# Kernel tuning notes

Measured on AMD Instinct MI355X. Metric: run time of the kernel, lower is better.

## Reference

```python
import jax, jax.numpy as jnp
import numpy as np
from functools import partial

N_QUBITS = 8
DEPTH = 2
INPUT_DIM = 128
HIDDEN_DIM = N_QUBITS  # required: hx = o * tanh(cx) elementwise
DIM = 2 ** N_QUBITS

# Z expectation matrix: ZMAT[k, i] = +1/-1 depending on bit of basis state k at wire i
# (wire 0 is the most-significant qubit, PennyLane convention)
_bits = ((np.arange(DIM)[:, None] >> (N_QUBITS - 1 - np.arange(N_QUBITS)[None, :])) & 1)
ZMAT = jnp.asarray(1.0 - 2.0 * _bits, dtype=jnp.float32)  # [2**n, n]


def _apply_1q(state, G, wire):
    """Apply 2x2 gate G ([2,2] shared or [B,2,2] batched) on `wire`."""
    B = state.shape[0]
    left, right = 2 ** wire, 2 ** (N_QUBITS - wire - 1)
    s = state.reshape(B, left, 2, right)
    if G.ndim == 2:
        s = jnp.einsum('ij,bljr->blir', G, s)
    else:
        s = jnp.einsum('bij,bljr->blir', G, s)
    return s.reshape(B, DIM)


def _apply_cnot(state, wire):
    """CNOT with control=wire, target=wire+1 (adjacent)."""
    B = state.shape[0]
    left, right = 2 ** wire, 2 ** (N_QUBITS - wire - 2)
    s = state.reshape(B, left, 2, 2, right)
    s = jnp.concatenate([s[:, :, :1], s[:, :, 1:, ::-1]], axis=2)
    return s.reshape(B, DIM)


def quantum_gate(angles, params):
    """angles: [B, n] RX rotation angles; params: [depth, n] RY angles.
    Returns [B, n] PauliZ expectations (exact statevector simulation)."""
    B = angles.shape[0]
    state = jnp.zeros((B, DIM), dtype=jnp.complex64).at[:, 0].set(1.0)
    # RX encoding layer (batched angles)
    c = jnp.cos(angles / 2).astype(jnp.complex64)
    s = (-1j) * jnp.sin(angles / 2).astype(jnp.complex64)
    for i in range(N_QUBITS):
        G = jnp.stack([jnp.stack([c[:, i], s[:, i]], -1),
                       jnp.stack([s[:, i], c[:, i]], -1)], -2)  # [B,2,2]
        state = _apply_1q(state, G, i)
    # variational layers: RY (shared params) + CNOT chain
    cp = jnp.cos(params / 2).astype(jnp.complex64)
    sp = jnp.sin(params / 2).astype(jnp.complex64)
    for d in range(DEPTH):
        for i in range(N_QUBITS):
            G = jnp.array([[1.0, 0.0], [0.0, 1.0]], jnp.complex64)
            G = jnp.stack([jnp.stack([cp[d, i], -sp[d, i]]),
                           jnp.stack([sp[d, i], cp[d, i]])])  # [2,2]
            state = _apply_1q(state, G, i)
        for i in range(N_QUBITS - 1):
            state = _apply_cnot(state, i)
    probs = (state.real ** 2 + state.imag ** 2)  # [B, 2**n]
    return probs @ ZMAT  # [B, n]


def setup_inputs() -> dict:
    key = jax.random.key(0)
    ks = jax.random.split(key, 13)
    T, B = 256, 1024
    cat = INPUT_DIM + HIDDEN_DIM
    lin_scale = 1.0 / np.sqrt(cat)
    d = {'inputs': jax.random.normal(ks[0], (T, B, INPUT_DIM), jnp.float32)}
    for idx, g in enumerate(['f', 'i', 'g', 'o']):
        d[f'W{g}'] = jax.random.uniform(ks[1 + 3 * idx], (N_QUBITS, cat), jnp.float32, -lin_scale, lin_scale)
        d[f'b{g}'] = jax.random.uniform(ks[2 + 3 * idx], (N_QUBITS,), jnp.float32, -lin_scale, lin_scale)
        d[f'P{g}'] = jax.random.normal(ks[3 + 3 * idx], (DEPTH, N_QUBITS), jnp.float32)
    return d


def reference(inputs, Wf, bf, Pf, Wi, bi, Pi, Wg, bg, Pg, Wo, bo, Po):
    T, B, _ = inputs.shape
    h0 = jnp.zeros((B, HIDDEN_DIM), inputs.dtype)
    c0 = jnp.zeros((B, HIDDEN_DIM), inputs.dtype)

    def step(carry, x):
        hx, cx = carry
        comb = jnp.concatenate([x, hx], axis=1)  # [B, input+hidden]
        f = jax.nn.sigmoid(quantum_gate(comb @ Wf.T + bf, Pf))
        i = jax.nn.sigmoid(quantum_gate(comb @ Wi.T + bi, Pi))
        g = jnp.tanh(quantum_gate(comb @ Wg.T + bg, Pg))
        o = jax.nn.sigmoid(quantum_gate(comb @ Wo.T + bo, Po))
        cx = f * cx + i * g
        hx = o * jnp.tanh(cx)
        return (hx, cx), hx

    (hx, cx), outputs = jax.lax.scan(step, (h0, c0), inputs)
    return outputs, (hx, cx)
```

## Files before the change

### kernel.cpp

```cpp
#include <hip/hip_runtime.h>
#include <math.h>

#define TS 256
#define BB 1024
#define NQ 8
#define INDIM 128
#define CATDIM 136
#define INV2PI 0.15915494309189535f
#define LOG2E  1.4426950408889634f

typedef float v2f __attribute__((ext_vector_type(2)));

__device__ __forceinline__ float dpp_xor1(float v) {
    return __int_as_float(__builtin_amdgcn_mov_dpp(__float_as_int(v), 0xB1, 0xF, 0xF, true));
}
__device__ __forceinline__ float dpp_xor2(float v) {
    return __int_as_float(__builtin_amdgcn_mov_dpp(__float_as_int(v), 0x4E, 0xF, 0xF, true));
}
__device__ __forceinline__ float dpp_xor8(float v) {
    return __int_as_float(__builtin_amdgcn_mov_dpp(__float_as_int(v), 0x128, 0xF, 0xF, true));
}
__device__ __forceinline__ float swz4(float v)  {
    return __int_as_float(__builtin_amdgcn_ds_swizzle(__float_as_int(v), 0x101F));
}
__device__ __forceinline__ float swz16(float v) {
    return __int_as_float(__builtin_amdgcn_ds_swizzle(__float_as_int(v), 0x401F));
}
__device__ __forceinline__ float swz20(float v) {
    return __int_as_float(__builtin_amdgcn_ds_swizzle(__float_as_int(v), 0x501F));
}
__device__ __forceinline__ float hw_sin(float x) { float r; asm("v_sin_f32 %0, %1" : "=v"(r) : "v"(x)); return r; }
__device__ __forceinline__ float hw_cos(float x) { float r; asm("v_cos_f32 %0, %1" : "=v"(r) : "v"(x)); return r; }
__device__ __forceinline__ float hw_exp(float x) { float r; asm("v_exp_f32 %0, %1" : "=v"(r) : "v"(x)); return r; }
__device__ __forceinline__ float hw_rcp(float x) { float r; asm("v_rcp_f32 %0, %1" : "=v"(r) : "v"(x)); return r; }
__device__ __forceinline__ v2f mk2(float x, float y) { v2f r; r.x = x; r.y = y; return r; }
__device__ __forceinline__ v2f pk_mul(v2f a, v2f b) {
    v2f d; asm("v_pk_mul_f32 %0, %1, %2" : "=v"(d) : "v"(a), "v"(b)); return d;
}
__device__ __forceinline__ v2f pk_fma(v2f a, v2f b, v2f c) {
    v2f d; asm("v_pk_fma_f32 %0, %1, %2, %3" : "=v"(d) : "v"(a), "v"(b), "v"(c)); return d;
}

__launch_bounds__(64, 1)
__attribute__((amdgpu_waves_per_eu(1, 1)))
__global__ void qlstm_f(const float* __restrict__ x,
    const float* __restrict__ Wf, const float* __restrict__ bf, const float* __restrict__ Pf,
    const float* __restrict__ Wi, const float* __restrict__ bi, const float* __restrict__ Pi,
    const float* __restrict__ Wg, const float* __restrict__ bg, const float* __restrict__ Pg,
    const float* __restrict__ Wo, const float* __restrict__ bo, const float* __restrict__ Po,
    float* __restrict__ out, float* __restrict__ hst, float* __restrict__ cst)
{
    const int lane = threadIdx.x;
    const int l0 = lane & 1, l1 = (lane >> 1) & 1, l3 = (lane >> 3) & 1;
    const int q = 4 * l0 + 2 * l1 + l3;
    const int g = ((lane >> 2) & 1) | ((lane >> 3) & 2);
    const int el2 = lane >> 5;
    const int b = blockIdx.x * 2 + el2;

    const float* W; const float* P; const float* bs;
    if (g == 0)      { W = Wf; P = Pf; bs = bf; }
    else if (g == 1) { W = Wi; P = Pi; bs = bi; }
    else if (g == 2) { W = Wg; P = Pg; bs = bg; }
    else             { W = Wo; P = Po; bs = bo; }

    float Chw[8], nSw[8], hsp0[8], cp0c[8];
    #pragma unroll
    for (int w = 0; w < 8; ++w) {
        float s1, c1, s0, c0;
        __sincosf(P[8 + w], &s1, &c1);
        __sincosf(P[w], &s0, &c0);
        Chw[w] = 0.5f * c1;
        nSw[w] = -s1;
        hsp0[w] = 0.5f * s0;
        cp0c[w] = c0;
    }

    v2f xw[8][8];
    #pragma unroll
    for (int j = 0; j < 8; ++j) {
        const float* Wj = W + j * CATDIM + 16 * q;
        #pragma unroll
        for (int p2 = 0; p2 < 4; ++p2) {
            float4 v = *(const float4*)(Wj + p2 * 4);
            xw[j][p2*2]   = mk2(INV2PI * v.x, INV2PI * v.y);
            xw[j][p2*2+1] = mk2(INV2PI * v.z, INV2PI * v.w);
        }
    }

    v2f whq[4];
    {
        const float* Wq = W + q * CATDIM + INDIM;
        #pragma unroll
        for (int p2 = 0; p2 < 4; ++p2)
            whq[p2] = mk2(INV2PI * Wq[q ^ (2 * p2)], INV2PI * Wq[q ^ (2 * p2 + 1)]);
    }
    const float bq = INV2PI * bs[q];

    const float kl = ((g == 2) ? 2.f : -1.f) * LOG2E;
    const float Aa = (g == 2) ? 1.f : 0.f;
    const float Bb = (g == 2) ? -1.f : 1.f;
    float sel[8];
    #pragma unroll
    for (int i = 0; i < 8; ++i) sel[i] = (q == i) ? kl : 0.f;

    float s0h = 0.f, s1h = 0.f, s2h = 0.f, s3h = 0.f;
    float s4h = 0.f, s5h = 0.f, s6h = 0.f, s7h = 0.f;
    float c_own = 0.f, hv = 0.f;

    const float* xptr = x + (size_t)b * INDIM + 16 * q;
    float4 xv0 = *(const float4*)(xptr);
    float4 xv1 = *(const float4*)(xptr + 4);
    float4 xv2 = *(const float4*)(xptr + 8);
    float4 xv3 = *(const float4*)(xptr + 12);
    xptr += (size_t)BB * INDIM;

    const bool emit = (lane & 0x14) == 0;
    float* optr = out + (size_t)b * NQ + q;

    #pragma unroll 2
    for (int t = 0; t < TS; ++t) {
        v2f xc[8] = { mk2(xv0.x, xv0.y), mk2(xv0.z, xv0.w),
                      mk2(xv1.x, xv1.y), mk2(xv1.z, xv1.w),
                      mk2(xv2.x, xv2.y), mk2(xv2.z, xv2.w),
                      mk2(xv3.x, xv3.y), mk2(xv3.z, xv3.w) };
        float pt[8];
        #pragma unroll
        for (int j = 0; j < 8; ++j) {
            v2f acc = pk_mul(xc[0], xw[j][0]);
            acc = pk_fma(xc[1], xw[j][1], acc);
            acc = pk_fma(xc[2], xw[j][2], acc);
            acc = pk_fma(xc[3], xw[j][3], acc);
            acc = pk_fma(xc[4], xw[j][4], acc);
            acc = pk_fma(xc[5], xw[j][5], acc);
            acc = pk_fma(xc[6], xw[j][6], acc);
            acc = pk_fma(xc[7], xw[j][7], acc);
            pt[j] = acc.x + acc.y;
        }

        {
            float4 xn0 = *(const float4*)(xptr);
            float4 xn1 = *(const float4*)(xptr + 4);
            float4 xn2 = *(const float4*)(xptr + 8);
            float4 xn3 = *(const float4*)(xptr + 12);
            xptr += (t < TS - 2) ? (size_t)BB * INDIM : 0;
            xv0 = xn0; xv1 = xn1; xv2 = xn2; xv3 = xn3;
        }

        {
            float s, r;
            s = l0 ? pt[0] : pt[4]; r = dpp_xor1(s); pt[0] = (l0 ? pt[4] : pt[0]) + r;
            s = l0 ? pt[1] : pt[5]; r = dpp_xor1(s); pt[1] = (l0 ? pt[5] : pt[1]) + r;
            s = l0 ? pt[2] : pt[6]; r = dpp_xor1(s); pt[2] = (l0 ? pt[6] : pt[2]) + r;
            s = l0 ? pt[3] : pt[7]; r = dpp_xor1(s); pt[3] = (l0 ? pt[7] : pt[3]) + r;
            s = l1 ? pt[0] : pt[2]; r = dpp_xor2(s); pt[0] = (l1 ? pt[2] : pt[0]) + r;
            s = l1 ? pt[1] : pt[3]; r = dpp_xor2(s); pt[1] = (l1 ? pt[3] : pt[1]) + r;
            s = l3 ? pt[0] : pt[1]; r = dpp_xor8(s); pt[0] = (l3 ? pt[1] : pt[0]) + r;
        }

        v2f hacc = pk_fma(mk2(s0h, s1h), whq[0], mk2(pt[0] + bq, 0.f));
        hacc = pk_fma(mk2(s2h, s3h), whq[1], hacc);
        hacc = pk_fma(mk2(s4h, s5h), whq[2], hacc);
        hacc = pk_fma(mk2(s6h, s7h), whq[3], hacc);
        float ang = hacc.x + hacc.y;

        float sa_own = hw_sin(ang);
        float ca_own = hw_cos(ang);

        float sa_0, sa_1, ca_0, ca_1;
        {
            float p = dpp_xor1(sa_own);
            sa_0 = l0 ? p : sa_own;  sa_1 = l0 ? sa_own : p;
            p = dpp_xor1(ca_own);
            ca_0 = l0 ? p : ca_own;  ca_1 = l0 ? ca_own : p;
        }
        float sa00, sa01, sa10, sa11, ca00, ca01, ca10, ca11;
        {
            float p0 = dpp_xor2(sa_0), p1 = dpp_xor2(sa_1);
            sa00 = l1 ? p0 : sa_0;  sa01 = l1 ? sa_0 : p0;
            sa10 = l1 ? p1 : sa_1;  sa11 = l1 ? sa_1 : p1;
            p0 = dpp_xor2(ca_0); p1 = dpp_xor2(ca_1);
            ca00 = l1 ? p0 : ca_0;  ca01 = l1 ? ca_0 : p0;
            ca10 = l1 ? p1 : ca_1;  ca11 = l1 ? ca_1 : p1;
        }
        float saw[8], caw[8];
        {
            float p;
            p = dpp_xor8(sa00); saw[0] = l3 ? p : sa00; saw[1] = l3 ? sa00 : p;
            p = dpp_xor8(sa01); saw[2] = l3 ? p : sa01; saw[3] = l3 ? sa01 : p;
            p = dpp_xor8(sa10); saw[4] = l3 ? p : sa10; saw[5] = l3 ? sa10 : p;
            p = dpp_xor8(sa11); saw[6] = l3 ? p : sa11; saw[7] = l3 ? sa11 : p;
            p = dpp_xor8(ca00); caw[0] = l3 ? p : ca00; caw[1] = l3 ? ca00 : p;
            p = dpp_xor8(ca01); caw[2] = l3 ? p : ca01; caw[3] = l3 ? ca01 : p;
            p = dpp_xor8(ca10); caw[4] = l3 ? p : ca10; caw[5] = l3 ? ca10 : p;
            p = dpp_xor8(ca11); caw[6] = l3 ? p : ca11; caw[7] = l3 ? ca11 : p;
        }

        float kE = 0.f;
        float d0, d1, zr, zi;
        {
            float AmB = cp0c[0] * caw[0];
            d0 = Chw[0] * (1.f + AmB);
            d1 = -(Chw[0] * (1.f - AmB));
            zr = nSw[0] * (hsp0[0] * caw[0]);
            zi = nSw[0] * (-0.5f * saw[0]);
        }
        #pragma unroll
        for (int w = 1; w < 8; ++w) {
            float gr = hsp0[w] * caw[w];
            float gi = -0.5f * saw[w];
            float AmB = cp0c[w] * caw[w];
            float sum = d0 + d1, dif = d0 - d1;
            float p = gr * zr, qv = gi * zi;
            float Ew = fmaf(4.f, p, sum);
            kE = fmaf(sel[w - 1], Ew, kE);
            float ad = AmB * dif;
            float e1 = sum + ad, e3 = sum - ad;
            float e2 = p - qv, e4 = p + qv;
            float T0 = fmaf(4.f, e2, e1);
            float T1 = fmaf(4.f, e4, e3);
            float f1 = fmaf(gr, sum, zr);
            float f3 = fmaf(AmB, zi, gi * dif);
            d0 = Chw[w] * T0;
            d1 = -(Chw[w] * T1);
            zr = nSw[w] * f1;
            zi = nSw[w] * f3;
        }
        {
            float E7 = (d0 + d1) + 2.f * zr;
            kE = fmaf(sel[7], E7, kE);
        }

        float y = hw_exp(kE);
        float a = fmaf(Aa, y, Bb) * hw_rcp(y + 1.f);

        float b4 = swz4(a);
        float b16 = swz16(a);
        float b20 = swz20(a);
        bool g1b = (g & 2) != 0;
        bool g0b = (g & 1) != 0;
        float e0 = g1b ? b16 : a;
        float e1s = g1b ? b20 : b4;
        float e2s = g1b ? a : b16;
        float e3s = g1b ? b4 : b20;
        float fv = g0b ? e1s : e0;
        float iv = g0b ? e0 : e1s;
        float gv = g0b ? e3s : e2s;
        float ov = g0b ? e2s : e3s;

        c_own = fmaf(fv, c_own, iv * gv);
        float e2c = hw_exp(c_own * (2.f * LOG2E));
        hv = ov * ((e2c - 1.f) * hw_rcp(e2c + 1.f));

        if (emit) *optr = hv;
        optr += (size_t)BB * NQ;

        s0h = hv;
        s4h = dpp_xor1(s0h);
        s2h = dpp_xor2(s0h);
        s6h = dpp_xor2(s4h);
        s1h = dpp_xor8(s0h);
        s5h = dpp_xor8(s4h);
        s3h = dpp_xor8(s2h);
        s7h = dpp_xor8(s6h);
    }

    if (emit) {
        hst[b * NQ + q] = hv;
        cst[b * NQ + q] = c_own;
    }
}

extern "C" void kernel_launch(void* const* d_in, const int* in_sizes, int n_in,
                              void* d_out, int out_size, void* d_ws, size_t ws_size,
                              hipStream_t stream) {
    const float* x  = (const float*)d_in[0];
    const float* Wf = (const float*)d_in[1];
    const float* bf = (const float*)d_in[2];
    const float* Pf = (const float*)d_in[3];
    const float* Wi = (const float*)d_in[4];
    const float* bi = (const float*)d_in[5];
    const float* Pi = (const float*)d_in[6];
    const float* Wg = (const float*)d_in[7];
    const float* bg = (const float*)d_in[8];
    const float* Pg = (const float*)d_in[9];
    const float* Wo = (const float*)d_in[10];
    const float* bo = (const float*)d_in[11];
    const float* Po = (const float*)d_in[12];

    float* out = (float*)d_out;
    float* hst = out + (size_t)TS * BB * NQ;
    float* cst = hst + (size_t)BB * NQ;

    qlstm_f<<<BB / 2, 64, 0, stream>>>(x, Wf, bf, Pf, Wi, bi, Pi,
                                       Wg, bg, Pg, Wo, bo, Po,
                                       out, hst, cst);
}
```

Baseline: 231.8 us.

## Use one batch row per wave with fp16 dot2 input projection

Each wave now handles a single batch element rather than two. The 128-wide input projection is split across both half-waves, with a cross-half shuffle to combine the partial sums. The input and weights are converted to packed fp16 and accumulated with v_dot2_f32_f16, which halves the projection instructions and register footprint per lane. This launches twice as many waves to shorten the serial per-step chain, but it adds a 32-lane shuffle per step and lowers input precision to fp16 with round-toward-zero conversion.

```diff
diff --git a/kernel.cpp b/kernel.cpp
--- a/kernel.cpp
+++ b/kernel.cpp
@@ -10,6 +10,7 @@
 #define LOG2E  1.4426950408889634f
 
 typedef float v2f __attribute__((ext_vector_type(2)));
+typedef __fp16 v2h __attribute__((ext_vector_type(2)));
 
 __device__ __forceinline__ float dpp_xor1(float v) {
     return __int_as_float(__builtin_amdgcn_mov_dpp(__float_as_int(v), 0xB1, 0xF, 0xF, true));
@@ -34,11 +35,11 @@
 __device__ __forceinline__ float hw_exp(float x) { float r; asm("v_exp_f32 %0, %1" : "=v"(r) : "v"(x)); return r; }
 __device__ __forceinline__ float hw_rcp(float x) { float r; asm("v_rcp_f32 %0, %1" : "=v"(r) : "v"(x)); return r; }
 __device__ __forceinline__ v2f mk2(float x, float y) { v2f r; r.x = x; r.y = y; return r; }
-__device__ __forceinline__ v2f pk_mul(v2f a, v2f b) {
-    v2f d; asm("v_pk_mul_f32 %0, %1, %2" : "=v"(d) : "v"(a), "v"(b)); return d;
-}
 __device__ __forceinline__ v2f pk_fma(v2f a, v2f b, v2f c) {
     v2f d; asm("v_pk_fma_f32 %0, %1, %2, %3" : "=v"(d) : "v"(a), "v"(b), "v"(c)); return d;
+}
+__device__ __forceinline__ float fdot2(v2h a, v2h b, float c) {
+    float d; asm("v_dot2_f32_f16 %0, %1, %2, %3" : "=v"(d) : "v"(a), "v"(b), "v"(c)); return d;
 }
 
 __launch_bounds__(64, 1)
@@ -54,8 +55,9 @@
     const int l0 = lane & 1, l1 = (lane >> 1) & 1, l3 = (lane >> 3) & 1;
     const int q = 4 * l0 + 2 * l1 + l3;
     const int g = ((lane >> 2) & 1) | ((lane >> 3) & 2);
-    const int el2 = lane >> 5;
-    const int b = blockIdx.x * 2 + el2;
+    const int k1 = lane >> 5;
+    const int b = blockIdx.x;
+    const int c = 8 * k1 + q;
 
     const float* W; const float* P; const float* bs;
     if (g == 0)      { W = Wf; P = Pf; bs = bf; }
@@ -75,16 +77,13 @@
         cp0c[w] = c0;
     }
 
-    v2f xw[8][8];
+    v2h xw[8][4];
     #pragma unroll
     for (int j = 0; j < 8; ++j) {
-        const float* Wj = W + j * CATDIM + 16 * q;
-        #pragma unroll
-        for (int p2 = 0; p2 < 4; ++p2) {
-            float4 v = *(const float4*)(Wj + p2 * 4);
-            xw[j][p2*2]   = mk2(INV2PI * v.x, INV2PI * v.y);
-            xw[j][p2*2+1] = mk2(INV2PI * v.z, INV2PI * v.w);
-        }
+        const float* Wj = W + j * CATDIM + 8 * c;
+        #pragma unroll
+        for (int p2 = 0; p2 < 4; ++p2)
+            xw[j][p2] = __builtin_amdgcn_cvt_pkrtz(INV2PI * Wj[2*p2], INV2PI * Wj[2*p2+1]);
     }
 
     v2f whq[4];
@@ -107,43 +106,40 @@
     float s4h = 0.f, s5h = 0.f, s6h = 0.f, s7h = 0.f;
     float c_own = 0.f, hv = 0.f;
 
-    const float* xptr = x + (size_t)b * INDIM + 16 * q;
-    float4 xv0 = *(const float4*)(xptr);
-    float4 xv1 = *(const float4*)(xptr + 4);
-    float4 xv2 = *(const float4*)(xptr + 8);
-    float4 xv3 = *(const float4*)(xptr + 12);
+    const float* xptr = x + (size_t)b * INDIM + 8 * c;
+    v2h xh[4];
+    {
+        float4 a0 = *(const float4*)(xptr);
+        float4 a1 = *(const float4*)(xptr + 4);
+        xh[0] = __builtin_amdgcn_cvt_pkrtz(a0.x, a0.y);
+        xh[1] = __builtin_amdgcn_cvt_pkrtz(a0.z, a0.w);
+        xh[2] = __builtin_amdgcn_cvt_pkrtz(a1.x, a1.y);
+        xh[3] = __builtin_amdgcn_cvt_pkrtz(a1.z, a1.w);
+    }
     xptr += (size_t)BB * INDIM;
 
-    const bool emit = (lane & 0x14) == 0;
+    const bool emit = (lane & 0x34) == 0;
     float* optr = out + (size_t)b * NQ + q;
 
-    #pragma unroll 2
     for (int t = 0; t < TS; ++t) {
-        v2f xc[8] = { mk2(xv0.x, xv0.y), mk2(xv0.z, xv0.w),
-                      mk2(xv1.x, xv1.y), mk2(xv1.z, xv1.w),
-                      mk2(xv2.x, xv2.y), mk2(xv2.z, xv2.w),
-                      mk2(xv3.x, xv3.y), mk2(xv3.z, xv3.w) };
         float pt[8];
         #pragma unroll
         for (int j = 0; j < 8; ++j) {
-            v2f acc = pk_mul(xc[0], xw[j][0]);
-            acc = pk_fma(xc[1], xw[j][1], acc);
-            acc = pk_fma(xc[2], xw[j][2], acc);
-            acc = pk_fma(xc[3], xw[j][3], acc);
-            acc = pk_fma(xc[4], xw[j][4], acc);
-            acc = pk_fma(xc[5], xw[j][5], acc);
-            acc = pk_fma(xc[6], xw[j][6], acc);
-            acc = pk_fma(xc[7], xw[j][7], acc);
-            pt[j] = acc.x + acc.y;
-        }
-
-        {
-            float4 xn0 = *(const float4*)(xptr);
-            float4 xn1 = *(const float4*)(xptr + 4);
-            float4 xn2 = *(const float4*)(xptr + 8);
-            float4 xn3 = *(const float4*)(xptr + 12);
+            float acc = fdot2(xh[0], xw[j][0], 0.f);
+            acc = fdot2(xh[1], xw[j][1], acc);
+            acc = fdot2(xh[2], xw[j][2], acc);
+            acc = fdot2(xh[3], xw[j][3], acc);
+            pt[j] = acc;
+        }
+
+        {
+            float4 a0 = *(const float4*)(xptr);
+            float4 a1 = *(const float4*)(xptr + 4);
             xptr += (t < TS - 2) ? (size_t)BB * INDIM : 0;
-            xv0 = xn0; xv1 = xn1; xv2 = xn2; xv3 = xn3;
+            xh[0] = __builtin_amdgcn_cvt_pkrtz(a0.x, a0.y);
+            xh[1] = __builtin_amdgcn_cvt_pkrtz(a0.z, a0.w);
+            xh[2] = __builtin_amdgcn_cvt_pkrtz(a1.x, a1.y);
+            xh[3] = __builtin_amdgcn_cvt_pkrtz(a1.z, a1.w);
         }
 
         {
@@ -155,6 +151,7 @@
             s = l1 ? pt[0] : pt[2]; r = dpp_xor2(s); pt[0] = (l1 ? pt[2] : pt[0]) + r;
             s = l1 ? pt[1] : pt[3]; r = dpp_xor2(s); pt[1] = (l1 ? pt[3] : pt[1]) + r;
             s = l3 ? pt[0] : pt[1]; r = dpp_xor8(s); pt[0] = (l3 ? pt[1] : pt[0]) + r;
+            pt[0] += __shfl_xor(pt[0], 32, 64);
         }
 
         v2f hacc = pk_fma(mk2(s0h, s1h), whq[0], mk2(pt[0] + bq, 0.f));
@@ -291,7 +288,7 @@
     float* hst = out + (size_t)TS * BB * NQ;
     float* cst = hst + (size_t)BB * NQ;
 
-    qlstm_f<<<BB / 2, 64, 0, stream>>>(x, Wf, bf, Pf, Wi, bi, Pi,
-                                       Wg, bg, Pg, Wo, bo, Po,
-                                       out, hst, cst);
-}
+    qlstm_f<<<BB, 64, 0, stream>>>(x, Wf, bf, Pf, Wi, bi, Pi,
+                                   Wg, bg, Pg, Wo, bo, Po,
+                                   out, hst, cst);
+}
```

Measured after the change: 236.6 us. 2.1% more time.
